# Performance work log

Hardware: AMD Instinct MI355X
Metric: run time of the kernel (lower is better)

The kernel has to match this reference:

```python
import jax, jax.numpy as jnp
import numpy as np

N = 100000          # number of active sparse points
GRID = 800          # coordinate grid extent (2D)
KS = 9              # 3x3 kernel offsets
C_IN = 24
C_HID = 144         # round(24 * 6)
C_OUT = 24
EPS = 1e-5


def _build_kernel_map():
    """Build MinkowskiEngine-style kernel map for a 3x3 stride-1 channelwise conv.
    Returns (in_idx, out_idx, off_id), each [KS*N] int32. Invalid (no neighbor)
    entries point to sentinel row N so the padded gather/scatter is a no-op."""
    rng = np.random.default_rng(0)
    flat = rng.choice(GRID * GRID, size=N, replace=False)  # unique 2D coords
    ys, xs = flat // GRID, flat % GRID
    coord_to_idx = -np.ones(GRID * GRID, dtype=np.int64)
    coord_to_idx[flat] = np.arange(N)
    in_chunks, out_chunks, off_chunks = [], [], []
    pts = np.arange(N, dtype=np.int64)
    k = 0
    for dy in (-1, 0, 1):
        for dx in (-1, 0, 1):
            ny, nx = ys + dy, xs + dx
            inside = (ny >= 0) & (ny < GRID) & (nx >= 0) & (nx < GRID)
            nflat = np.clip(ny, 0, GRID - 1) * GRID + np.clip(nx, 0, GRID - 1)
            nidx = np.where(inside, coord_to_idx[nflat], -1)
            valid = nidx >= 0
            in_chunks.append(np.where(valid, nidx, N))
            out_chunks.append(np.where(valid, pts, N))
            off_chunks.append(np.full(N, k, dtype=np.int64))
            k += 1
    in_idx = np.concatenate(in_chunks).astype(np.int32)
    out_idx = np.concatenate(out_chunks).astype(np.int32)
    off_id = np.concatenate(off_chunks).astype(np.int32)
    return in_idx, out_idx, off_id


def setup_inputs() -> dict:
    key = jax.random.key(0)
    ks = jax.random.split(key, 4)
    in_idx, out_idx, off_id = _build_kernel_map()
    return {
        "feats": jax.random.normal(ks[0], (N, C_IN), jnp.float32),
        "w1": jax.random.normal(ks[1], (C_IN, C_HID), jnp.float32) * 0.1,
        "g1": jnp.ones((C_HID,), jnp.float32),
        "b1": jnp.zeros((C_HID,), jnp.float32),
        "w2": jax.random.normal(ks[2], (KS, C_HID), jnp.float32) * 0.1,
        "g2": jnp.ones((C_HID,), jnp.float32),
        "b2": jnp.zeros((C_HID,), jnp.float32),
        "w3": jax.random.normal(ks[3], (C_HID, C_OUT), jnp.float32) * 0.1,
        "g3": jnp.ones((C_OUT,), jnp.float32),
        "b3": jnp.zeros((C_OUT,), jnp.float32),
        "in_idx": jnp.asarray(in_idx),
        "out_idx": jnp.asarray(out_idx),
        "off_id": jnp.asarray(off_id),
    }


def _bn(x, g, b):
    # MinkowskiBatchNorm forward (training mode): per-channel stats over points
    m = jnp.mean(x, axis=0)
    v = jnp.var(x, axis=0)
    return (x - m) * jax.lax.rsqrt(v + EPS) * g + b


def _relu6(x):
    return jnp.clip(x, 0.0, 6.0)


def _channelwise_conv3x3(x, w2, in_idx, out_idx, off_id):
    # gather-multiply-scatter: out[p, c] = sum_k w2[k, c] * x[nbr_k(p), c]
    xp = jnp.concatenate([x, jnp.zeros((1, x.shape[1]), x.dtype)], axis=0)  # sentinel row
    contrib = xp[in_idx] * w2[off_id]                     # [KS*N, C_HID]
    out = jnp.zeros((N + 1, x.shape[1]), x.dtype).at[out_idx].add(contrib)
    return out[:N]


def reference(feats, w1, g1, b1, w2, g2, b2, w3, g3, b3, in_idx, out_idx, off_id):
    x = _relu6(_bn(feats @ w1, g1, b1))                   # 1x1 expand
    x = _relu6(_bn(_channelwise_conv3x3(x, w2, in_idx, out_idx, off_id), g2, b2))
    x = _bn(x @ w3, g3, b3)                               # 1x1 project
    return x + feats                                      # residual (in==out, stride==1)
```

## Files before the change

### kernel.cpp

```cpp
#include <hip/hip_runtime.h>
#include <hip/hip_fp16.h>

#define N_PTS 100000
#define KSZ 9
#define C_IN 24
#define C_HID 144
#define C_OUT 24
#define EPSV 1e-5f

#define X1N_B 0ull
#define X2_B  28800512ull
#define ST_B  57600512ull
#define Y3_B  0ull

#define MU1_F  0
#define M1_F   32
#define SUM2_F 640
#define SQ2_F  800
#define SUM3_F 960
#define SQ3_F  992
#define ST_FLOATS 1024

typedef float f4v __attribute__((ext_vector_type(4)));

__device__ inline float4 f4z() { return make_float4(0.f, 0.f, 0.f, 0.f); }
__device__ inline float4 f4_fma_s(float s, float4 b, float4 c) {
    return make_float4(fmaf(s, b.x, c.x), fmaf(s, b.y, c.y),
                       fmaf(s, b.z, c.z), fmaf(s, b.w, c.w));
}
__device__ inline float clamp6(float x) { return fminf(fmaxf(x, 0.f), 6.f); }

__global__ void k_init(char* wsb) {
    int t = threadIdx.x;
    float* STF = (float*)(wsb + ST_B);
    for (int i = t; i < ST_FLOATS; i += 256) STF[i] = 0.f;
    float* sent = (float*)(wsb + X1N_B + (size_t)N_PTS * (C_HID * 2));
    if (t < 72) sent[t] = 0.f;
}

__global__ void k_moments(const float* __restrict__ feats, char* __restrict__ wsb) {
    int t = threadIdx.x;
    float* STF = (float*)(wsb + ST_B);
    int len = (N_PTS + gridDim.x - 1) / gridDim.x;
    int r0 = blockIdx.x * len;
    int r1 = min(r0 + len, N_PTS);
    if (t >= 600) return;
    float a = 0.f;
    if (t < 576) {
        int i = t / 24, j = t % 24;
#pragma unroll 4
        for (int r = r0; r < r1; r++)
            a = fmaf(feats[(size_t)r * 24 + i], feats[(size_t)r * 24 + j], a);
        atomicAdd(&STF[M1_F + t], a);
    } else {
        int k = t - 576;
#pragma unroll 4
        for (int r = r0; r < r1; r++) a += feats[(size_t)r * 24 + k];
        atomicAdd(&STF[MU1_F + k], a);
    }
}

__global__ void __launch_bounds__(576, 5)
k_gemm1(const float* __restrict__ feats, const float* __restrict__ w1,
        const float* __restrict__ g1, const float* __restrict__ b1,
        char* __restrict__ wsb) {
    __shared__ float scs[C_HID], shs[C_HID];
    float* STF = (float*)(wsb + ST_B);
    int t = threadIdx.x;
    if (t < C_HID) {
        float wc[C_IN];
#pragma unroll
        for (int k = 0; k < C_IN; k++) wc[k] = w1[k * C_HID + t];
        const float invN = 1.f / (float)N_PTS;
        float mean = 0.f;
#pragma unroll
        for (int k = 0; k < C_IN; k++) mean = fmaf(STF[MU1_F + k], wc[k], mean);
        mean *= invN;
        float e2 = 0.f;
        for (int i = 0; i < C_IN; i++) {
            float s = 0.f;
#pragma unroll
            for (int j = 0; j < C_IN; j++) s = fmaf(STF[M1_F + i * 24 + j], wc[j], s);
            e2 = fmaf(wc[i], s, e2);
        }
        e2 *= invN;
        float var = e2 - mean * mean;
        float s1 = g1[t] * rsqrtf(var + EPSV);
        scs[t] = s1;
        shs[t] = b1[t] - mean * s1;
    }
    __syncthreads();
    int c = t % C_HID, pg = t / C_HID;
    float sc = scs[c];
    float sh = shs[c];
    float wreg[C_IN];
#pragma unroll
    for (int k = 0; k < C_IN; k++) wreg[k] = w1[k * C_HID + c] * sc;
    __half* x1h = (__half*)(wsb + X1N_B);
    for (int p = blockIdx.x * 4 + pg; p < N_PTS; p += gridDim.x * 4) {
        const float4* fr = (const float4*)(feats + (size_t)p * C_IN);
        float acc = sh;
#pragma unroll
        for (int q = 0; q < 6; q++) {
            float4 f = fr[q];
            acc = fmaf(f.x, wreg[4 * q + 0], acc);
            acc = fmaf(f.y, wreg[4 * q + 1], acc);
            acc = fmaf(f.z, wreg[4 * q + 2], acc);
            acc = fmaf(f.w, wreg[4 * q + 3], acc);
        }
        x1h[(size_t)p * C_HID + c] = __float2half_rn(clamp6(acc));
    }
}

__global__ void k_conv(const float* __restrict__ w2, const int* __restrict__ in_idx,
                       char* __restrict__ wsb) {
    __shared__ float w2s[KSZ * C_HID];
    __shared__ float lsum[C_HID], lsq[C_HID];
    float* STF = (float*)(wsb + ST_B);
    int t = threadIdx.x;
    for (int e = t; e < KSZ * C_HID; e += 256) w2s[e] = w2[e];
    if (t < C_HID) { lsum[t] = 0.f; lsq[t] = 0.f; }
    __syncthreads();
    const __half* x1h = (const __half*)(wsb + X1N_B);
    __half* x2h = (__half*)(wsb + X2_B);
    const bool act = t < 252;
    int pt = t / 18, g = t % 18, c0 = g * 8;
    float rs[8], rq[8];
#pragma unroll
    for (int j = 0; j < 8; j++) { rs[j] = 0.f; rq[j] = 0.f; }
    const int nChunks = (N_PTS + 13) / 14;
    int ch = (int)blockIdx.x;
    int p = ch * 14 + pt;
    bool ok = act && p < N_PTS;
    int idxs[KSZ];
#pragma unroll
    for (int k = 0; k < KSZ; k++) idxs[k] = ok ? in_idx[k * N_PTS + p] : N_PTS;
    while (ch < nChunks) {
        float4 vv[KSZ];
#pragma unroll
        for (int k = 0; k < KSZ; k++)
            vv[k] = *(const float4*)(x1h + (size_t)idxs[k] * C_HID + c0);
        int chn = ch + (int)gridDim.x;
        int pn = chn * 14 + pt;
        bool okn = act && chn < nChunks && pn < N_PTS;
        int idxn[KSZ];
#pragma unroll
        for (int k = 0; k < KSZ; k++) idxn[k] = okn ? in_idx[k * N_PTS + pn] : N_PTS;
        float acc[8];
#pragma unroll
        for (int j = 0; j < 8; j++) acc[j] = 0.f;
#pragma unroll
        for (int k = 0; k < KSZ; k++) {
            union { float4 f; __half2 h[4]; } u;
            u.f = vv[k];
#pragma unroll
            for (int jj = 0; jj < 4; jj++) {
                float2 x = __half22float2(u.h[jj]);
                acc[2 * jj]     = fmaf(w2s[k * C_HID + c0 + 2 * jj],     x.x, acc[2 * jj]);
                acc[2 * jj + 1] = fmaf(w2s[k * C_HID + c0 + 2 * jj + 1], x.y, acc[2 * jj + 1]);
            }
        }
        if (ok) {
            union { f4v f; __half2 h[4]; } o;
#pragma unroll
            for (int jj = 0; jj < 4; jj++)
                o.h[jj] = __float22half2_rn(make_float2(acc[2 * jj], acc[2 * jj + 1]));
            __builtin_nontemporal_store(o.f, (f4v*)(x2h + (size_t)p * C_HID + c0));
#pragma unroll
            for (int j = 0; j < 8; j++) {
                rs[j] += acc[j];
                rq[j] = fmaf(acc[j], acc[j], rq[j]);
            }
        }
        ch = chn; p = pn; ok = okn;
#pragma unroll
        for (int k = 0; k < KSZ; k++) idxs[k] = idxn[k];
    }
    if (act) {
#pragma unroll
        for (int j = 0; j < 8; j++) {
            atomicAdd(&lsum[c0 + j], rs[j]);
            atomicAdd(&lsq[c0 + j], rq[j]);
        }
    }
    __syncthreads();
    if (t < C_HID) {
        atomicAdd(&STF[SUM2_F + t], lsum[t]);
        atomicAdd(&STF[SQ2_F + t], lsq[t]);
    }
}

__global__ void k_gemm2(const float* __restrict__ w3, const float* __restrict__ g2,
                        const float* __restrict__ b2, char* __restrict__ wsb) {
    __shared__ float4 w3s[C_HID * 6];
    __shared__ float4 sc2v[C_HID / 4], sh2v[C_HID / 4];
    float* STF = (float*)(wsb + ST_B);
    int t = threadIdx.x;
    for (int e = t; e < C_HID * 6; e += 256) w3s[e] = ((const float4*)w3)[e];
    if (t < C_HID) {
        const float invN = 1.f / (float)N_PTS;
        float mean = STF[SUM2_F + t] * invN;
        float var = STF[SQ2_F + t] * invN - mean * mean;
        float s = g2[t] * rsqrtf(var + EPSV);
        ((float*)sc2v)[t] = s;
        ((float*)sh2v)[t] = b2[t] - mean * s;
    }
    __syncthreads();
    int r = blockIdx.x * 256 + t;
    if (r >= N_PTS) return;
    const float4* x2v = (const float4*)(wsb + X2_B + (size_t)r * (C_HID * 2));
    float4 a[6];
#pragma unroll
    for (int c4 = 0; c4 < 6; c4++) a[c4] = f4z();
#pragma unroll 6
    for (int h8 = 0; h8 < 18; h8++) {
        union { float4 f; __half2 h[4]; } u;
        u.f = x2v[h8];
        float4 s0 = sc2v[2 * h8], s1 = sc2v[2 * h8 + 1];
        float4 b0 = sh2v[2 * h8], b1 = sh2v[2 * h8 + 1];
        float2 x0 = __half22float2(u.h[0]);
        float2 x1 = __half22float2(u.h[1]);
        float2 x2 = __half22float2(u.h[2]);
        float2 x3 = __half22float2(u.h[3]);
        float xs[8];
        xs[0] = clamp6(fmaf(x0.x, s0.x, b0.x));
        xs[1] = clamp6(fmaf(x0.y, s0.y, b0.y));
        xs[2] = clamp6(fmaf(x1.x, s0.z, b0.z));
        xs[3] = clamp6(fmaf(x1.y, s0.w, b0.w));
        xs[4] = clamp6(fmaf(x2.x, s1.x, b1.x));
        xs[5] = clamp6(fmaf(x2.y, s1.y, b1.y));
        xs[6] = clamp6(fmaf(x3.x, s1.z, b1.z));
        xs[7] = clamp6(fmaf(x3.y, s1.w, b1.w));
#pragma unroll
        for (int j = 0; j < 8; j++) {
            int h = h8 * 8 + j;
#pragma unroll
            for (int c4 = 0; c4 < 6; c4++)
                a[c4] = f4_fma_s(xs[j], w3s[h * 6 + c4], a[c4]);
        }
    }
    float4* y3v = (float4*)(wsb + Y3_B) + (size_t)r * 6;
#pragma unroll
    for (int c4 = 0; c4 < 6; c4++) y3v[c4] = a[c4];
}

__global__ void k_red3(char* __restrict__ wsb) {
    int t = threadIdx.x;
    const float* y3 = (const float*)(wsb + Y3_B);
    float* STF = (float*)(wsb + ST_B);
    float rs = 0.f, rq = 0.f;
    const int total = N_PTS * C_OUT;
    for (int e = blockIdx.x * 192 + t; e < total; e += gridDim.x * 192) {
        float v = y3[e];
        rs += v;
        rq = fmaf(v, v, rq);
    }
    __shared__ float ls[192], lq[192];
    ls[t] = rs; lq[t] = rq;
    __syncthreads();
    if (t < C_OUT) {
        float s = 0.f, q = 0.f;
        for (int u = t; u < 192; u += C_OUT) { s += ls[u]; q += lq[u]; }
        atomicAdd(&STF[SUM3_F + t], s);
        atomicAdd(&STF[SQ3_F + t], q);
    }
}

__global__ void k_out(const float* __restrict__ feats, const float* __restrict__ g3,
                      const float* __restrict__ b3, const char* __restrict__ wsb,
                      float* __restrict__ out) {
    __shared__ float s3[C_OUT], h3[C_OUT];
    const float* STF = (const float*)(wsb + ST_B);
    int t = threadIdx.x;
    if (t < C_OUT) {
        const float invN = 1.f / (float)N_PTS;
        float mean = STF[SUM3_F + t] * invN;
        float var = STF[SQ3_F + t] * invN - mean * mean;
        float s = g3[t] * rsqrtf(var + EPSV);
        s3[t] = s;
        h3[t] = b3[t] - mean * s;
    }
    __syncthreads();
    int tau = blockIdx.x * 256 + t;
    if (tau >= N_PTS * 6) return;
    int c = (tau % 6) * 4;
    float4 y = ((const float4*)(wsb + Y3_B))[tau];
    float4 f = ((const float4*)feats)[tau];
    float4 o;
    o.x = fmaf(y.x, s3[c + 0], h3[c + 0]) + f.x;
    o.y = fmaf(y.y, s3[c + 1], h3[c + 1]) + f.y;
    o.z = fmaf(y.z, s3[c + 2], h3[c + 2]) + f.z;
    o.w = fmaf(y.w, s3[c + 3], h3[c + 3]) + f.w;
    ((float4*)out)[tau] = o;
}

extern "C" void kernel_launch(void* const* d_in, const int* in_sizes, int n_in,
                              void* d_out, int out_size, void* d_ws, size_t ws_size,
                              hipStream_t stream) {
    const float* feats = (const float*)d_in[0];
    const float* w1 = (const float*)d_in[1];
    const float* g1 = (const float*)d_in[2];
    const float* b1 = (const float*)d_in[3];
    const float* w2 = (const float*)d_in[4];
    const float* g2 = (const float*)d_in[5];
    const float* b2 = (const float*)d_in[6];
    const float* w3 = (const float*)d_in[7];
    const float* g3 = (const float*)d_in[8];
    const float* b3 = (const float*)d_in[9];
    const int* in_idx = (const int*)d_in[10];
    char* wsb = (char*)d_ws;
    float* out = (float*)d_out;

    hipLaunchKernelGGL(k_init, dim3(1), dim3(256), 0, stream, wsb);
    hipLaunchKernelGGL(k_moments, dim3(256), dim3(640), 0, stream, feats, wsb);
    hipLaunchKernelGGL(k_gemm1, dim3(1024), dim3(576), 0, stream, feats, w1, g1, b1, wsb);
    hipLaunchKernelGGL(k_conv, dim3(2048), dim3(256), 0, stream, w2, in_idx, wsb);
    hipLaunchKernelGGL(k_gemm2, dim3((N_PTS + 255) / 256), dim3(256), 0, stream, w3, g2, b2, wsb);
    hipLaunchKernelGGL(k_red3, dim3(512), dim3(192), 0, stream, wsb);
    hipLaunchKernelGGL(k_out, dim3((N_PTS * 6 + 255) / 256), dim3(256), 0, stream,
                       feats, g3, b3, wsb, out);
}
```

Baseline: 292.6 us.

## Fuse all stages into one cooperative persistent kernel with grid syncs

```diff
diff --git a/kernel.cpp b/kernel.cpp
--- a/kernel.cpp
+++ b/kernel.cpp
@@ -1,5 +1,8 @@
 #include <hip/hip_runtime.h>
 #include <hip/hip_fp16.h>
+#include <hip/hip_cooperative_groups.h>
+
+namespace cg = cooperative_groups;
 
 #define N_PTS 100000
 #define KSZ 9
@@ -7,20 +10,30 @@
 #define C_HID 144
 #define C_OUT 24
 #define EPSV 1e-5f
+#define NB 768
+#define BT 256
+#define NCH14 ((N_PTS + 13) / 14)
+#define NPAIR (N_PTS / 2)
 
 #define X1N_B 0ull
 #define X2_B  28800512ull
 #define ST_B  57600512ull
 #define Y3_B  0ull
 
-#define MU1_F  0
-#define M1_F   32
-#define SUM2_F 640
-#define SQ2_F  800
-#define SUM3_F 960
-#define SQ3_F  992
-#define ST_FLOATS 1024
-
+#define MSUM1 0
+#define MSQ1  160
+#define MSUM2 320
+#define MSQ2  480
+#define MSUM3 640
+#define MSQ3  672
+#define FB_MU1  0
+#define FB_M1   32
+#define FB_SUM2 640
+#define FB_SQ2  800
+#define FB_SUM3 960
+#define FB_SQ3  992
+
+typedef float f2v __attribute__((ext_vector_type(2)));
 typedef float f4v __attribute__((ext_vector_type(4)));
 
 __device__ inline float4 f4z() { return make_float4(0.f, 0.f, 0.f, 0.f); }
@@ -30,12 +43,277 @@
 }
 __device__ inline float clamp6(float x) { return fminf(fmaxf(x, 0.f), 6.f); }
 
-__global__ void k_init(char* wsb) {
-    int t = threadIdx.x;
+__global__ void __launch_bounds__(BT, 4)
+mega(const float* __restrict__ feats, const float* __restrict__ w1,
+     const float* __restrict__ g1, const float* __restrict__ b1,
+     const float* __restrict__ w2, const float* __restrict__ g2,
+     const float* __restrict__ b2, const float* __restrict__ w3,
+     const float* __restrict__ g3, const float* __restrict__ b3,
+     const int* __restrict__ in_idx, char* __restrict__ wsb,
+     float* __restrict__ out) {
+    cg::grid_group gg = cg::this_grid();
+    __shared__ __align__(16) float smem[3936];
+    const int t = threadIdx.x;
+    const int bid = blockIdx.x;
     float* STF = (float*)(wsb + ST_B);
-    for (int i = t; i < ST_FLOATS; i += 256) STF[i] = 0.f;
-    float* sent = (float*)(wsb + X1N_B + (size_t)N_PTS * (C_HID * 2));
-    if (t < 72) sent[t] = 0.f;
+    __half* x1h = (__half*)(wsb + X1N_B);
+    __half* x2h = (__half*)(wsb + X2_B);
+
+    {
+        for (int e = t; e < 864; e += BT) ((float4*)smem)[e] = ((const float4*)w1)[e];
+        if (t < C_HID) { smem[3456 + t] = 0.f; smem[3600 + t] = 0.f; }
+        if (bid == 0 && t < 72)
+            ((unsigned int*)(x1h + (size_t)N_PTS * C_HID))[t] = 0xFC00FC00u;
+        __syncthreads();
+        const float4* w1s = (const float4*)smem;
+        bool act = t < 252;
+        int pt = t / 36, g = t % 36;
+        float4 rs = f4z(), rq = f4z();
+        for (int ch = bid; ch < NCH14; ch += NB) {
+            int pp = ch * 7 + pt;
+            if (act && pp < NPAIR) {
+                int p0 = pp * 2, p1 = p0 + 1;
+                const float4* fa = (const float4*)(feats + (size_t)p0 * C_IN);
+                const float4* fb = (const float4*)(feats + (size_t)p1 * C_IN);
+                float4 A = f4z(), Bv = f4z();
+#pragma unroll
+                for (int q = 0; q < 6; q++) {
+                    float4 x = fa[q], y = fb[q];
+                    float4 w0 = w1s[(4 * q + 0) * 36 + g];
+                    float4 w1r = w1s[(4 * q + 1) * 36 + g];
+                    float4 w2r = w1s[(4 * q + 2) * 36 + g];
+                    float4 w3r = w1s[(4 * q + 3) * 36 + g];
+                    A = f4_fma_s(x.x, w0, A);  Bv = f4_fma_s(y.x, w0, Bv);
+                    A = f4_fma_s(x.y, w1r, A); Bv = f4_fma_s(y.y, w1r, Bv);
+                    A = f4_fma_s(x.z, w2r, A); Bv = f4_fma_s(y.z, w2r, Bv);
+                    A = f4_fma_s(x.w, w3r, A); Bv = f4_fma_s(y.w, w3r, Bv);
+                }
+                union { f2v f; __half2 h2[2]; } ua, ub;
+                ua.h2[0] = __float22half2_rn(make_float2(A.x, A.y));
+                ua.h2[1] = __float22half2_rn(make_float2(A.z, A.w));
+                ub.h2[0] = __float22half2_rn(make_float2(Bv.x, Bv.y));
+                ub.h2[1] = __float22half2_rn(make_float2(Bv.z, Bv.w));
+                *(f2v*)(x1h + (size_t)p0 * C_HID + g * 4) = ua.f;
+                *(f2v*)(x1h + (size_t)p1 * C_HID + g * 4) = ub.f;
+                rs.x += A.x + Bv.x; rs.y += A.y + Bv.y;
+                rs.z += A.z + Bv.z; rs.w += A.w + Bv.w;
+                rq.x += A.x * A.x + Bv.x * Bv.x; rq.y += A.y * A.y + Bv.y * Bv.y;
+                rq.z += A.z * A.z + Bv.z * Bv.z; rq.w += A.w * A.w + Bv.w * Bv.w;
+            }
+        }
+        if (act) {
+            atomicAdd(&smem[3456 + g * 4 + 0], rs.x);
+            atomicAdd(&smem[3456 + g * 4 + 1], rs.y);
+            atomicAdd(&smem[3456 + g * 4 + 2], rs.z);
+            atomicAdd(&smem[3456 + g * 4 + 3], rs.w);
+            atomicAdd(&smem[3600 + g * 4 + 0], rq.x);
+            atomicAdd(&smem[3600 + g * 4 + 1], rq.y);
+            atomicAdd(&smem[3600 + g * 4 + 2], rq.z);
+            atomicAdd(&smem[3600 + g * 4 + 3], rq.w);
+        }
+        __syncthreads();
+        if (t < C_HID) {
+            atomicAdd(&STF[MSUM1 + t], smem[3456 + t]);
+            atomicAdd(&STF[MSQ1 + t], smem[3600 + t]);
+        }
+    }
+    __threadfence();
+    gg.sync();
+
+    {
+        for (int e = t; e < KSZ * C_HID; e += BT) smem[e] = w2[e];
+        if (t < C_HID) { smem[1296 + t] = 0.f; smem[1440 + t] = 0.f; }
+        bool act = t < 252;
+        int pt = t / 18, g = t % 18, c0 = g * 8;
+        float sc[8], sh[8];
+        const float invN = 1.f / (float)N_PTS;
+#pragma unroll
+        for (int j = 0; j < 8; j++) {
+            int c = c0 + j;
+            float mean = STF[MSUM1 + c] * invN;
+            float var = STF[MSQ1 + c] * invN - mean * mean;
+            float s = g1[c] * rsqrtf(var + EPSV);
+            sc[j] = s;
+            sh[j] = b1[c] - mean * s;
+        }
+        __syncthreads();
+        float rs[8], rq[8];
+#pragma unroll
+        for (int j = 0; j < 8; j++) { rs[j] = 0.f; rq[j] = 0.f; }
+        int ch = bid;
+        int p = ch * 14 + pt;
+        bool ok = act && p < N_PTS;
+        int idxs[KSZ];
+#pragma unroll
+        for (int k = 0; k < KSZ; k++) idxs[k] = ok ? in_idx[k * N_PTS + p] : N_PTS;
+        while (ch < NCH14) {
+            float4 vv[KSZ];
+#pragma unroll
+            for (int k = 0; k < KSZ; k++)
+                vv[k] = *(const float4*)(x1h + (size_t)idxs[k] * C_HID + c0);
+            int chn = ch + NB;
+            int pn = chn * 14 + pt;
+            bool okn = act && chn < NCH14 && pn < N_PTS;
+            int idxn[KSZ];
+#pragma unroll
+            for (int k = 0; k < KSZ; k++) idxn[k] = okn ? in_idx[k * N_PTS + pn] : N_PTS;
+            float acc[8];
+#pragma unroll
+            for (int j = 0; j < 8; j++) acc[j] = 0.f;
+#pragma unroll
+            for (int k = 0; k < KSZ; k++) {
+                union { float4 f; __half2 h[4]; } u;
+                u.f = vv[k];
+#pragma unroll
+                for (int jj = 0; jj < 4; jj++) {
+                    float2 x = __half22float2(u.h[jj]);
+                    float xa = clamp6(fmaf(x.x, sc[2 * jj], sh[2 * jj]));
+                    float xb = clamp6(fmaf(x.y, sc[2 * jj + 1], sh[2 * jj + 1]));
+                    acc[2 * jj]     = fmaf(smem[k * C_HID + c0 + 2 * jj], xa, acc[2 * jj]);
+                    acc[2 * jj + 1] = fmaf(smem[k * C_HID + c0 + 2 * jj + 1], xb, acc[2 * jj + 1]);
+                }
+            }
+            if (ok) {
+                union { f4v f; __half2 h[4]; } o;
+#pragma unroll
+                for (int jj = 0; jj < 4; jj++)
+                    o.h[jj] = __float22half2_rn(make_float2(acc[2 * jj], acc[2 * jj + 1]));
+                __builtin_nontemporal_store(o.f, (f4v*)(x2h + (size_t)p * C_HID + c0));
+            }
+#pragma unroll
+            for (int j = 0; j < 8; j++) {
+                rs[j] += acc[j];
+                rq[j] = fmaf(acc[j], acc[j], rq[j]);
+            }
+            ch = chn; p = pn; ok = okn;
+#pragma unroll
+            for (int k = 0; k < KSZ; k++) idxs[k] = idxn[k];
+        }
+        if (act) {
+#pragma unroll
+            for (int j = 0; j < 8; j++) {
+                atomicAdd(&smem[1296 + c0 + j], rs[j]);
+                atomicAdd(&smem[1440 + c0 + j], rq[j]);
+            }
+        }
+        __syncthreads();
+        if (t < C_HID) {
+            atomicAdd(&STF[MSUM2 + t], smem[1296 + t]);
+            atomicAdd(&STF[MSQ2 + t], smem[1440 + t]);
+        }
+    }
+    __threadfence();
+    gg.sync();
+
+    {
+        bool blkact = (bid * BT < N_PTS);
+        if (blkact) {
+            for (int e = t; e < 864; e += BT) ((float4*)smem)[e] = ((const float4*)w3)[e];
+            if (t < C_HID) {
+                const float invN = 1.f / (float)N_PTS;
+                float mean = STF[MSUM2 + t] * invN;
+                float var = STF[MSQ2 + t] * invN - mean * mean;
+                float s = g2[t] * rsqrtf(var + EPSV);
+                smem[3456 + t] = s;
+                smem[3600 + t] = b2[t] - mean * s;
+            }
+            __syncthreads();
+            int p = bid * BT + t;
+            bool ok = p < N_PTS;
+            float4 a[6];
+#pragma unroll
+            for (int c4 = 0; c4 < 6; c4++) a[c4] = f4z();
+            if (ok) {
+                const float4* xr = (const float4*)(x2h + (size_t)p * C_HID);
+                const float4* sc2 = (const float4*)(smem + 3456);
+                const float4* sh2 = (const float4*)(smem + 3600);
+                const float4* w3s = (const float4*)smem;
+#pragma unroll 3
+                for (int h8 = 0; h8 < 18; h8++) {
+                    union { float4 f; __half2 h[4]; } u;
+                    u.f = xr[h8];
+                    float4 s0 = sc2[2 * h8], s1 = sc2[2 * h8 + 1];
+                    float4 b0 = sh2[2 * h8], b1v = sh2[2 * h8 + 1];
+                    float2 x0 = __half22float2(u.h[0]);
+                    float2 x1 = __half22float2(u.h[1]);
+                    float2 x2 = __half22float2(u.h[2]);
+                    float2 x3 = __half22float2(u.h[3]);
+                    float xs[8];
+                    xs[0] = clamp6(fmaf(x0.x, s0.x, b0.x));
+                    xs[1] = clamp6(fmaf(x0.y, s0.y, b0.y));
+                    xs[2] = clamp6(fmaf(x1.x, s0.z, b0.z));
+                    xs[3] = clamp6(fmaf(x1.y, s0.w, b0.w));
+                    xs[4] = clamp6(fmaf(x2.x, s1.x, b1v.x));
+                    xs[5] = clamp6(fmaf(x2.y, s1.y, b1v.y));
+                    xs[6] = clamp6(fmaf(x3.x, s1.z, b1v.z));
+                    xs[7] = clamp6(fmaf(x3.y, s1.w, b1v.w));
+#pragma unroll
+                    for (int j = 0; j < 8; j++) {
+                        int h = h8 * 8 + j;
+#pragma unroll
+                        for (int c4 = 0; c4 < 6; c4++)
+                            a[c4] = f4_fma_s(xs[j], w3s[h * 6 + c4], a[c4]);
+                    }
+                }
+                float4* y3v = (float4*)(wsb + Y3_B) + (size_t)p * 6;
+#pragma unroll
+                for (int c4 = 0; c4 < 6; c4++) y3v[c4] = a[c4];
+            }
+            int wv = t >> 6, ln = t & 63;
+#pragma unroll
+            for (int c4 = 0; c4 < 6; c4++) {
+                float4 s = a[c4];
+                float4 q = make_float4(s.x * s.x, s.y * s.y, s.z * s.z, s.w * s.w);
+#pragma unroll
+                for (int m = 1; m < 64; m <<= 1) {
+                    s.x += __shfl_xor(s.x, m); s.y += __shfl_xor(s.y, m);
+                    s.z += __shfl_xor(s.z, m); s.w += __shfl_xor(s.w, m);
+                    q.x += __shfl_xor(q.x, m); q.y += __shfl_xor(q.y, m);
+                    q.z += __shfl_xor(q.z, m); q.w += __shfl_xor(q.w, m);
+                }
+                if (ln == 0) {
+                    int base = 3744 + wv * 48 + c4 * 4;
+                    smem[base + 0] = s.x; smem[base + 1] = s.y;
+                    smem[base + 2] = s.z; smem[base + 3] = s.w;
+                    smem[base + 24 + 0] = q.x; smem[base + 24 + 1] = q.y;
+                    smem[base + 24 + 2] = q.z; smem[base + 24 + 3] = q.w;
+                }
+            }
+            __syncthreads();
+            if (t < 48) {
+                float v = smem[3744 + t] + smem[3744 + 48 + t] +
+                          smem[3744 + 96 + t] + smem[3744 + 144 + t];
+                if (t < 24) atomicAdd(&STF[MSUM3 + t], v);
+                else        atomicAdd(&STF[MSQ3 + t - 24], v);
+            }
+        }
+    }
+    __threadfence();
+    gg.sync();
+
+    {
+        if (t < C_OUT) {
+            const float invN = 1.f / (float)N_PTS;
+            float mean = STF[MSUM3 + t] * invN;
+            float var = STF[MSQ3 + t] * invN - mean * mean;
+            float s = g3[t] * rsqrtf(var + EPSV);
+            smem[t] = s;
+            smem[32 + t] = b3[t] - mean * s;
+        }
+        __syncthreads();
+        const float4* s3v = (const float4*)smem;
+        const float4* h3v = (const float4*)(smem + 32);
+        const int T = N_PTS * 6;
+        for (int tau = bid * BT + t; tau < T; tau += NB * BT) {
+            int c4 = tau % 6;
+            float4 y = ((const float4*)(wsb + Y3_B))[tau];
+            float4 f = ((const float4*)feats)[tau];
+            float4 s = s3v[c4], h = h3v[c4];
+            ((float4*)out)[tau] = make_float4(
+                fmaf(y.x, s.x, h.x) + f.x, fmaf(y.y, s.y, h.y) + f.y,
+                fmaf(y.z, s.z, h.z) + f.z, fmaf(y.w, s.w, h.w) + f.w);
+        }
+    }
 }
 
 __global__ void k_moments(const float* __restrict__ feats, char* __restrict__ wsb) {
@@ -51,12 +329,12 @@
 #pragma unroll 4
         for (int r = r0; r < r1; r++)
             a = fmaf(feats[(size_t)r * 24 + i], feats[(size_t)r * 24 + j], a);
-        atomicAdd(&STF[M1_F + t], a);
+        atomicAdd(&STF[FB_M1 + t], a);
     } else {
         int k = t - 576;
 #pragma unroll 4
         for (int r = r0; r < r1; r++) a += feats[(size_t)r * 24 + k];
-        atomicAdd(&STF[MU1_F + k], a);
+        atomicAdd(&STF[FB_MU1 + k], a);
     }
 }
 
@@ -74,13 +352,13 @@
         const float invN = 1.f / (float)N_PTS;
         float mean = 0.f;
 #pragma unroll
-        for (int k = 0; k < C_IN; k++) mean = fmaf(STF[MU1_F + k], wc[k], mean);
+        for (int k = 0; k < C_IN; k++) mean = fmaf(STF[FB_MU1 + k], wc[k], mean);
         mean *= invN;
         float e2 = 0.f;
         for (int i = 0; i < C_IN; i++) {
             float s = 0.f;
 #pragma unroll
-            for (int j = 0; j < C_IN; j++) s = fmaf(STF[M1_F + i * 24 + j], wc[j], s);
+            for (int j = 0; j < C_IN; j++) s = fmaf(STF[FB_M1 + i * 24 + j], wc[j], s);
             e2 = fmaf(wc[i], s, e2);
         }
         e2 *= invN;
@@ -112,8 +390,8 @@
     }
 }
 
-__global__ void k_conv(const float* __restrict__ w2, const int* __restrict__ in_idx,
-                       char* __restrict__ wsb) {
+__global__ void k_conv_fb(const float* __restrict__ w2, const int* __restrict__ in_idx,
+                          char* __restrict__ wsb) {
     __shared__ float w2s[KSZ * C_HID];
     __shared__ float lsum[C_HID], lsq[C_HID];
     float* STF = (float*)(wsb + ST_B);
@@ -128,21 +406,20 @@
     float rs[8], rq[8];
 #pragma unroll
     for (int j = 0; j < 8; j++) { rs[j] = 0.f; rq[j] = 0.f; }
-    const int nChunks = (N_PTS + 13) / 14;
     int ch = (int)blockIdx.x;
     int p = ch * 14 + pt;
     bool ok = act && p < N_PTS;
     int idxs[KSZ];
 #pragma unroll
     for (int k = 0; k < KSZ; k++) idxs[k] = ok ? in_idx[k * N_PTS + p] : N_PTS;
-    while (ch < nChunks) {
+    while (ch < NCH14) {
         float4 vv[KSZ];
 #pragma unroll
         for (int k = 0; k < KSZ; k++)
             vv[k] = *(const float4*)(x1h + (size_t)idxs[k] * C_HID + c0);
         int chn = ch + (int)gridDim.x;
         int pn = chn * 14 + pt;
-        bool okn = act && chn < nChunks && pn < N_PTS;
+        bool okn = act && chn < NCH14 && pn < N_PTS;
         int idxn[KSZ];
 #pragma unroll
         for (int k = 0; k < KSZ; k++) idxn[k] = okn ? in_idx[k * N_PTS + pn] : N_PTS;
@@ -151,12 +428,12 @@
         for (int j = 0; j < 8; j++) acc[j] = 0.f;
 #pragma unroll
         for (int k = 0; k < KSZ; k++) {
-            union { float4 f; __half2 h[4]; } u;
+            union { float4 f; __half2 h[2][2]; } u;
             u.f = vv[k];
 #pragma unroll
             for (int jj = 0; jj < 4; jj++) {
-                float2 x = __half22float2(u.h[jj]);
-                acc[2 * jj]     = fmaf(w2s[k * C_HID + c0 + 2 * jj],     x.x, acc[2 * jj]);
+                float2 x = __half22float2(u.h[jj >> 1][jj & 1]);
+                acc[2 * jj]     = fmaf(w2s[k * C_HID + c0 + 2 * jj], x.x, acc[2 * jj]);
                 acc[2 * jj + 1] = fmaf(w2s[k * C_HID + c0 + 2 * jj + 1], x.y, acc[2 * jj + 1]);
             }
         }
@@ -166,11 +443,11 @@
             for (int jj = 0; jj < 4; jj++)
                 o.h[jj] = __float22half2_rn(make_float2(acc[2 * jj], acc[2 * jj + 1]));
             __builtin_nontemporal_store(o.f, (f4v*)(x2h + (size_t)p * C_HID + c0));
-#pragma unroll
-            for (int j = 0; j < 8; j++) {
-                rs[j] += acc[j];
-                rq[j] = fmaf(acc[j], acc[j], rq[j]);
-            }
+        }
+#pragma unroll
+        for (int j = 0; j < 8; j++) {
+            rs[j] += acc[j];
+            rq[j] = fmaf(acc[j], acc[j], rq[j]);
         }
         ch = chn; p = pn; ok = okn;
 #pragma unroll
@@ -185,8 +462,8 @@
     }
     __syncthreads();
     if (t < C_HID) {
-        atomicAdd(&STF[SUM2_F + t], lsum[t]);
-        atomicAdd(&STF[SQ2_F + t], lsq[t]);
+        atomicAdd(&STF[FB_SUM2 + t], lsum[t]);
+        atomicAdd(&STF[FB_SQ2 + t], lsq[t]);
     }
 }
 
@@ -194,75 +471,82 @@
                         const float* __restrict__ b2, char* __restrict__ wsb) {
     __shared__ float4 w3s[C_HID * 6];
     __shared__ float4 sc2v[C_HID / 4], sh2v[C_HID / 4];
+    __shared__ float red[192];
     float* STF = (float*)(wsb + ST_B);
     int t = threadIdx.x;
     for (int e = t; e < C_HID * 6; e += 256) w3s[e] = ((const float4*)w3)[e];
     if (t < C_HID) {
         const float invN = 1.f / (float)N_PTS;
-        float mean = STF[SUM2_F + t] * invN;
-        float var = STF[SQ2_F + t] * invN - mean * mean;
+        float mean = STF[FB_SUM2 + t] * invN;
+        float var = STF[FB_SQ2 + t] * invN - mean * mean;
         float s = g2[t] * rsqrtf(var + EPSV);
         ((float*)sc2v)[t] = s;
         ((float*)sh2v)[t] = b2[t] - mean * s;
     }
     __syncthreads();
     int r = blockIdx.x * 256 + t;
-    if (r >= N_PTS) return;
-    const float4* x2v = (const float4*)(wsb + X2_B + (size_t)r * (C_HID * 2));
+    bool ok = r < N_PTS;
     float4 a[6];
 #pragma unroll
     for (int c4 = 0; c4 < 6; c4++) a[c4] = f4z();
-#pragma unroll 6
-    for (int h8 = 0; h8 < 18; h8++) {
-        union { float4 f; __half2 h[4]; } u;
-        u.f = x2v[h8];
-        float4 s0 = sc2v[2 * h8], s1 = sc2v[2 * h8 + 1];
-        float4 b0 = sh2v[2 * h8], b1 = sh2v[2 * h8 + 1];
-        float2 x0 = __half22float2(u.h[0]);
-        float2 x1 = __half22float2(u.h[1]);
-        float2 x2 = __half22float2(u.h[2]);
-        float2 x3 = __half22float2(u.h[3]);
-        float xs[8];
-        xs[0] = clamp6(fmaf(x0.x, s0.x, b0.x));
-        xs[1] = clamp6(fmaf(x0.y, s0.y, b0.y));
-        xs[2] = clamp6(fmaf(x1.x, s0.z, b0.z));
-        xs[3] = clamp6(fmaf(x1.y, s0.w, b0.w));
-        xs[4] = clamp6(fmaf(x2.x, s1.x, b1.x));
-        xs[5] = clamp6(fmaf(x2.y, s1.y, b1.y));
-        xs[6] = clamp6(fmaf(x3.x, s1.z, b1.z));
-        xs[7] = clamp6(fmaf(x3.y, s1.w, b1.w));
-#pragma unroll
-        for (int j = 0; j < 8; j++) {
-            int h = h8 * 8 + j;
-#pragma unroll
-            for (int c4 = 0; c4 < 6; c4++)
-                a[c4] = f4_fma_s(xs[j], w3s[h * 6 + c4], a[c4]);
-        }
-    }
-    float4* y3v = (float4*)(wsb + Y3_B) + (size_t)r * 6;
-#pragma unroll
-    for (int c4 = 0; c4 < 6; c4++) y3v[c4] = a[c4];
-}
-
-__global__ void k_red3(char* __restrict__ wsb) {
-    int t = threadIdx.x;
-    const float* y3 = (const float*)(wsb + Y3_B);
-    float* STF = (float*)(wsb + ST_B);
-    float rs = 0.f, rq = 0.f;
-    const int total = N_PTS * C_OUT;
-    for (int e = blockIdx.x * 192 + t; e < total; e += gridDim.x * 192) {
-        float v = y3[e];
-        rs += v;
-        rq = fmaf(v, v, rq);
-    }
-    __shared__ float ls[192], lq[192];
-    ls[t] = rs; lq[t] = rq;
+    if (ok) {
+        const float4* x2v = (const float4*)(wsb + X2_B + (size_t)r * (C_HID * 2));
+#pragma unroll 3
+        for (int h8 = 0; h8 < 18; h8++) {
+            union { float4 f; __half2 h[4]; } u;
+            u.f = x2v[h8];
+            float4 s0 = sc2v[2 * h8], s1 = sc2v[2 * h8 + 1];
+            float4 b0 = sh2v[2 * h8], b1v = sh2v[2 * h8 + 1];
+            float2 x0 = __half22float2(u.h[0]);
+            float2 x1 = __half22float2(u.h[1]);
+            float2 x2 = __half22float2(u.h[2]);
+            float2 x3 = __half22float2(u.h[3]);
+            float xs[8];
+            xs[0] = clamp6(fmaf(x0.x, s0.x, b0.x));
+            xs[1] = clamp6(fmaf(x0.y, s0.y, b0.y));
+            xs[2] = clamp6(fmaf(x1.x, s0.z, b0.z));
+            xs[3] = clamp6(fmaf(x1.y, s0.w, b0.w));
+            xs[4] = clamp6(fmaf(x2.x, s1.x, b1v.x));
+            xs[5] = clamp6(fmaf(x2.y, s1.y, b1v.y));
+            xs[6] = clamp6(fmaf(x3.x, s1.z, b1v.z));
+            xs[7] = clamp6(fmaf(x3.y, s1.w, b1v.w));
+#pragma unroll
+            for (int j = 0; j < 8; j++) {
+                int h = h8 * 8 + j;
+#pragma unroll
+                for (int c4 = 0; c4 < 6; c4++)
+                    a[c4] = f4_fma_s(xs[j], w3s[h * 6 + c4], a[c4]);
+            }
+        }
+        float4* y3v = (float4*)(wsb + Y3_B) + (size_t)r * 6;
+#pragma unroll
+        for (int c4 = 0; c4 < 6; c4++) y3v[c4] = a[c4];
+    }
+    int wv = t >> 6, ln = t & 63;
+#pragma unroll
+    for (int c4 = 0; c4 < 6; c4++) {
+        float4 s = a[c4];
+        float4 q = make_float4(s.x * s.x, s.y * s.y, s.z * s.z, s.w * s.w);
+#pragma unroll
+        for (int m = 1; m < 64; m <<= 1) {
+            s.x += __shfl_xor(s.x, m); s.y += __shfl_xor(s.y, m);
+            s.z += __shfl_xor(s.z, m); s.w += __shfl_xor(s.w, m);
+            q.x += __shfl_xor(q.x, m); q.y += __shfl_xor(q.y, m);
+            q.z += __shfl_xor(q.z, m); q.w += __shfl_xor(q.w, m);
+        }
+        if (ln == 0) {
+            int base = wv * 48 + c4 * 4;
+            red[base + 0] = s.x; red[base + 1] = s.y;
+            red[base + 2] = s.z; red[base + 3] = s.w;
+            red[base + 24 + 0] = q.x; red[base + 24 + 1] = q.y;
+            red[base + 24 + 2] = q.z; red[base + 24 + 3] = q.w;
+        }
+    }
     __syncthreads();
-    if (t < C_OUT) {
-        float s = 0.f, q = 0.f;
-        for (int u = t; u < 192; u += C_OUT) { s += ls[u]; q += lq[u]; }
-        atomicAdd(&STF[SUM3_F + t], s);
-        atomicAdd(&STF[SQ3_F + t], q);
+    if (t < 48) {
+        float v = red[t] + red[48 + t] + red[96 + t] + red[144 + t];
+        if (t < 24) atomicAdd(&STF[FB_SUM3 + t], v);
+        else        atomicAdd(&STF[FB_SQ3 + t - 24], v);
     }
 }
 
@@ -274,8 +558,8 @@
     int t = threadIdx.x;
     if (t < C_OUT) {
         const float invN = 1.f / (float)N_PTS;
-        float mean = STF[SUM3_F + t] * invN;
-        float var = STF[SQ3_F + t] * invN - mean * mean;
+        float mean = STF[FB_SUM3 + t] * invN;
+        float var = STF[FB_SQ3 + t] * invN - mean * mean;
         float s = g3[t] * rsqrtf(var + EPSV);
         s3[t] = s;
         h3[t] = b3[t] - mean * s;
@@ -311,12 +595,37 @@
     char* wsb = (char*)d_ws;
     float* out = (float*)d_out;
 
-    hipLaunchKernelGGL(k_init, dim3(1), dim3(256), 0, stream, wsb);
-    hipLaunchKernelGGL(k_moments, dim3(256), dim3(640), 0, stream, feats, wsb);
-    hipLaunchKernelGGL(k_gemm1, dim3(1024), dim3(576), 0, stream, feats, w1, g1, b1, wsb);
-    hipLaunchKernelGGL(k_conv, dim3(2048), dim3(256), 0, stream, w2, in_idx, wsb);
-    hipLaunchKernelGGL(k_gemm2, dim3((N_PTS + 255) / 256), dim3(256), 0, stream, w3, g2, b2, wsb);
-    hipLaunchKernelGGL(k_red3, dim3(512), dim3(192), 0, stream, wsb);
-    hipLaunchKernelGGL(k_out, dim3((N_PTS * 6 + 255) / 256), dim3(256), 0, stream,
-                       feats, g3, b3, wsb, out);
-}
+    (void)hipMemsetAsync(wsb + ST_B, 0, 4096, stream);
+    (void)hipMemsetAsync(wsb + (size_t)N_PTS * C_HID * 2, 0, C_HID * 2, stream);
+
+    static int coop_ok = -1;
+    if (coop_ok < 0) {
+        int nblk = 0, ncu = 0, dev = 0;
+        (void)hipGetDevice(&dev);
+        hipError_t e1 = hipOccupancyMaxActiveBlocksPerMultiprocessor(
+            &nblk, (const void*)mega, BT, 0);
+        hipError_t e2 = hipDeviceGetAttribute(
+            &ncu, hipDeviceAttributeMultiprocessorCount, dev);
+        coop_ok = (e1 == hipSuccess && e2 == hipSuccess && nblk * ncu >= NB) ? 1 : 0;
+    }
+
+    bool did_coop = false;
+    if (coop_ok) {
+        void* args[] = {(void*)&feats, (void*)&w1, (void*)&g1, (void*)&b1,
+                        (void*)&w2, (void*)&g2, (void*)&b2, (void*)&w3,
+                        (void*)&g3, (void*)&b3, (void*)&in_idx, (void*)&wsb,
+                        (void*)&out};
+        hipError_t e = hipLaunchCooperativeKernel((const void*)mega, dim3(NB), dim3(BT),
+                                                  args, 0, stream);
+        did_coop = (e == hipSuccess);
+    }
+    if (!did_coop) {
+        hipLaunchKernelGGL(k_moments, dim3(256), dim3(640), 0, stream, feats, wsb);
+        hipLaunchKernelGGL(k_gemm1, dim3(1024), dim3(576), 0, stream, feats, w1, g1, b1, wsb);
+        hipLaunchKernelGGL(k_conv_fb, dim3(2048), dim3(256), 0, stream, w2, in_idx, wsb);
+        hipLaunchKernelGGL(k_gemm2, dim3((N_PTS + 255) / 256), dim3(256), 0, stream,
+                           w3, g2, b2, wsb);
+        hipLaunchKernelGGL(k_out, dim3((N_PTS * 6 + 255) / 256), dim3(256), 0, stream,
+                           feats, g3, b3, wsb, out);
+    }
+}
```

Result: slower. 313.6 us (+7.2%).

## Defer BN1 into conv gather, fuse output stats into gemm2, drop moment kernels

Applied to the files above, without the earlier changes.

```diff
diff --git a/kernel.cpp b/kernel.cpp
--- a/kernel.cpp
+++ b/kernel.cpp
@@ -7,20 +7,22 @@
 #define C_HID 144
 #define C_OUT 24
 #define EPSV 1e-5f
+#define NCH14 ((N_PTS + 13) / 14)
+#define NPAIR (N_PTS / 2)
 
 #define X1N_B 0ull
 #define X2_B  28800512ull
 #define ST_B  57600512ull
 #define Y3_B  0ull
 
-#define MU1_F  0
-#define M1_F   32
-#define SUM2_F 640
-#define SQ2_F  800
-#define SUM3_F 960
-#define SQ3_F  992
-#define ST_FLOATS 1024
-
+#define MSUM1 0
+#define MSQ1  160
+#define MSUM2 320
+#define MSQ2  480
+#define MSUM3 640
+#define MSQ3  672
+
+typedef float f2v __attribute__((ext_vector_type(2)));
 typedef float f4v __attribute__((ext_vector_type(4)));
 
 __device__ inline float4 f4z() { return make_float4(0.f, 0.f, 0.f, 0.f); }
@@ -30,89 +32,74 @@
 }
 __device__ inline float clamp6(float x) { return fminf(fmaxf(x, 0.f), 6.f); }
 
-__global__ void k_init(char* wsb) {
-    int t = threadIdx.x;
+__global__ void __launch_bounds__(256)
+k_gemm1(const float* __restrict__ feats, const float* __restrict__ w1,
+        char* __restrict__ wsb) {
+    __shared__ __align__(16) float smem[3744];
     float* STF = (float*)(wsb + ST_B);
-    for (int i = t; i < ST_FLOATS; i += 256) STF[i] = 0.f;
-    float* sent = (float*)(wsb + X1N_B + (size_t)N_PTS * (C_HID * 2));
-    if (t < 72) sent[t] = 0.f;
-}
-
-__global__ void k_moments(const float* __restrict__ feats, char* __restrict__ wsb) {
-    int t = threadIdx.x;
-    float* STF = (float*)(wsb + ST_B);
-    int len = (N_PTS + gridDim.x - 1) / gridDim.x;
-    int r0 = blockIdx.x * len;
-    int r1 = min(r0 + len, N_PTS);
-    if (t >= 600) return;
-    float a = 0.f;
-    if (t < 576) {
-        int i = t / 24, j = t % 24;
-#pragma unroll 4
-        for (int r = r0; r < r1; r++)
-            a = fmaf(feats[(size_t)r * 24 + i], feats[(size_t)r * 24 + j], a);
-        atomicAdd(&STF[M1_F + t], a);
-    } else {
-        int k = t - 576;
-#pragma unroll 4
-        for (int r = r0; r < r1; r++) a += feats[(size_t)r * 24 + k];
-        atomicAdd(&STF[MU1_F + k], a);
-    }
-}
-
-__global__ void __launch_bounds__(576, 5)
-k_gemm1(const float* __restrict__ feats, const float* __restrict__ w1,
-        const float* __restrict__ g1, const float* __restrict__ b1,
-        char* __restrict__ wsb) {
-    __shared__ float scs[C_HID], shs[C_HID];
-    float* STF = (float*)(wsb + ST_B);
-    int t = threadIdx.x;
+    __half* x1h = (__half*)(wsb + X1N_B);
+    const int t = threadIdx.x;
+    const int bid = blockIdx.x;
+    for (int e = t; e < 864; e += 256) ((float4*)smem)[e] = ((const float4*)w1)[e];
+    if (t < C_HID) { smem[3456 + t] = 0.f; smem[3600 + t] = 0.f; }
+    if (bid == 0 && t < 72)
+        ((unsigned int*)(x1h + (size_t)N_PTS * C_HID))[t] = 0xFC00FC00u;
+    __syncthreads();
+    const float4* w1s = (const float4*)smem;
+    bool act = t < 252;
+    int pt = t / 36, g = t % 36;
+    float4 rs = f4z(), rq = f4z();
+    for (int ch = bid; ch < NCH14; ch += (int)gridDim.x) {
+        int pp = ch * 7 + pt;
+        if (act && pp < NPAIR) {
+            int p0 = pp * 2, p1 = p0 + 1;
+            const float4* fa = (const float4*)(feats + (size_t)p0 * C_IN);
+            const float4* fb = (const float4*)(feats + (size_t)p1 * C_IN);
+            float4 A = f4z(), Bv = f4z();
+#pragma unroll
+            for (int q = 0; q < 6; q++) {
+                float4 x = fa[q], y = fb[q];
+                float4 w0 = w1s[(4 * q + 0) * 36 + g];
+                float4 w1r = w1s[(4 * q + 1) * 36 + g];
+                float4 w2r = w1s[(4 * q + 2) * 36 + g];
+                float4 w3r = w1s[(4 * q + 3) * 36 + g];
+                A = f4_fma_s(x.x, w0, A);  Bv = f4_fma_s(y.x, w0, Bv);
+                A = f4_fma_s(x.y, w1r, A); Bv = f4_fma_s(y.y, w1r, Bv);
+                A = f4_fma_s(x.z, w2r, A); Bv = f4_fma_s(y.z, w2r, Bv);
+                A = f4_fma_s(x.w, w3r, A); Bv = f4_fma_s(y.w, w3r, Bv);
+            }
+            union { f2v f; __half2 h2[2]; } ua, ub;
+            ua.h2[0] = __float22half2_rn(make_float2(A.x, A.y));
+            ua.h2[1] = __float22half2_rn(make_float2(A.z, A.w));
+            ub.h2[0] = __float22half2_rn(make_float2(Bv.x, Bv.y));
+            ub.h2[1] = __float22half2_rn(make_float2(Bv.z, Bv.w));
+            *(f2v*)(x1h + (size_t)p0 * C_HID + g * 4) = ua.f;
+            *(f2v*)(x1h + (size_t)p1 * C_HID + g * 4) = ub.f;
+            rs.x += A.x + Bv.x; rs.y += A.y + Bv.y;
+            rs.z += A.z + Bv.z; rs.w += A.w + Bv.w;
+            rq.x += A.x * A.x + Bv.x * Bv.x; rq.y += A.y * A.y + Bv.y * Bv.y;
+            rq.z += A.z * A.z + Bv.z * Bv.z; rq.w += A.w * A.w + Bv.w * Bv.w;
+        }
+    }
+    if (act) {
+        atomicAdd(&smem[3456 + g * 4 + 0], rs.x);
+        atomicAdd(&smem[3456 + g * 4 + 1], rs.y);
+        atomicAdd(&smem[3456 + g * 4 + 2], rs.z);
+        atomicAdd(&smem[3456 + g * 4 + 3], rs.w);
+        atomicAdd(&smem[3600 + g * 4 + 0], rq.x);
+        atomicAdd(&smem[3600 + g * 4 + 1], rq.y);
+        atomicAdd(&smem[3600 + g * 4 + 2], rq.z);
+        atomicAdd(&smem[3600 + g * 4 + 3], rq.w);
+    }
+    __syncthreads();
     if (t < C_HID) {
-        float wc[C_IN];
-#pragma unroll
-        for (int k = 0; k < C_IN; k++) wc[k] = w1[k * C_HID + t];
-        const float invN = 1.f / (float)N_PTS;
-        float mean = 0.f;
-#pragma unroll
-        for (int k = 0; k < C_IN; k++) mean = fmaf(STF[MU1_F + k], wc[k], mean);
-        mean *= invN;
-        float e2 = 0.f;
-        for (int i = 0; i < C_IN; i++) {
-            float s = 0.f;
-#pragma unroll
-            for (int j = 0; j < C_IN; j++) s = fmaf(STF[M1_F + i * 24 + j], wc[j], s);
-            e2 = fmaf(wc[i], s, e2);
-        }
-        e2 *= invN;
-        float var = e2 - mean * mean;
-        float s1 = g1[t] * rsqrtf(var + EPSV);
-        scs[t] = s1;
-        shs[t] = b1[t] - mean * s1;
-    }
-    __syncthreads();
-    int c = t % C_HID, pg = t / C_HID;
-    float sc = scs[c];
-    float sh = shs[c];
-    float wreg[C_IN];
-#pragma unroll
-    for (int k = 0; k < C_IN; k++) wreg[k] = w1[k * C_HID + c] * sc;
-    __half* x1h = (__half*)(wsb + X1N_B);
-    for (int p = blockIdx.x * 4 + pg; p < N_PTS; p += gridDim.x * 4) {
-        const float4* fr = (const float4*)(feats + (size_t)p * C_IN);
-        float acc = sh;
-#pragma unroll
-        for (int q = 0; q < 6; q++) {
-            float4 f = fr[q];
-            acc = fmaf(f.x, wreg[4 * q + 0], acc);
-            acc = fmaf(f.y, wreg[4 * q + 1], acc);
-            acc = fmaf(f.z, wreg[4 * q + 2], acc);
-            acc = fmaf(f.w, wreg[4 * q + 3], acc);
-        }
-        x1h[(size_t)p * C_HID + c] = __float2half_rn(clamp6(acc));
-    }
-}
-
-__global__ void k_conv(const float* __restrict__ w2, const int* __restrict__ in_idx,
+        atomicAdd(&STF[MSUM1 + t], smem[3456 + t]);
+        atomicAdd(&STF[MSQ1 + t], smem[3600 + t]);
+    }
+}
+
+__global__ void k_conv(const float* __restrict__ w2, const float* __restrict__ g1,
+                       const float* __restrict__ b1, const int* __restrict__ in_idx,
                        char* __restrict__ wsb) {
     __shared__ float w2s[KSZ * C_HID];
     __shared__ float lsum[C_HID], lsq[C_HID];
@@ -120,29 +107,41 @@
     int t = threadIdx.x;
     for (int e = t; e < KSZ * C_HID; e += 256) w2s[e] = w2[e];
     if (t < C_HID) { lsum[t] = 0.f; lsq[t] = 0.f; }
+    const bool act = t < 252;
+    int pt = t / 18, g = t % 18, c0 = g * 8;
+    float sc[8], sh[8];
+    {
+        const float invN = 1.f / (float)N_PTS;
+#pragma unroll
+        for (int j = 0; j < 8; j++) {
+            int c = c0 + j;
+            float mean = STF[MSUM1 + c] * invN;
+            float var = STF[MSQ1 + c] * invN - mean * mean;
+            float s = g1[c] * rsqrtf(var + EPSV);
+            sc[j] = s;
+            sh[j] = b1[c] - mean * s;
+        }
+    }
     __syncthreads();
     const __half* x1h = (const __half*)(wsb + X1N_B);
     __half* x2h = (__half*)(wsb + X2_B);
-    const bool act = t < 252;
-    int pt = t / 18, g = t % 18, c0 = g * 8;
     float rs[8], rq[8];
 #pragma unroll
     for (int j = 0; j < 8; j++) { rs[j] = 0.f; rq[j] = 0.f; }
-    const int nChunks = (N_PTS + 13) / 14;
     int ch = (int)blockIdx.x;
     int p = ch * 14 + pt;
     bool ok = act && p < N_PTS;
     int idxs[KSZ];
 #pragma unroll
     for (int k = 0; k < KSZ; k++) idxs[k] = ok ? in_idx[k * N_PTS + p] : N_PTS;
-    while (ch < nChunks) {
+    while (ch < NCH14) {
         float4 vv[KSZ];
 #pragma unroll
         for (int k = 0; k < KSZ; k++)
             vv[k] = *(const float4*)(x1h + (size_t)idxs[k] * C_HID + c0);
         int chn = ch + (int)gridDim.x;
         int pn = chn * 14 + pt;
-        bool okn = act && chn < nChunks && pn < N_PTS;
+        bool okn = act && chn < NCH14 && pn < N_PTS;
         int idxn[KSZ];
 #pragma unroll
         for (int k = 0; k < KSZ; k++) idxn[k] = okn ? in_idx[k * N_PTS + pn] : N_PTS;
@@ -156,8 +155,10 @@
 #pragma unroll
             for (int jj = 0; jj < 4; jj++) {
                 float2 x = __half22float2(u.h[jj]);
-                acc[2 * jj]     = fmaf(w2s[k * C_HID + c0 + 2 * jj],     x.x, acc[2 * jj]);
-                acc[2 * jj + 1] = fmaf(w2s[k * C_HID + c0 + 2 * jj + 1], x.y, acc[2 * jj + 1]);
+                float xa = clamp6(fmaf(x.x, sc[2 * jj], sh[2 * jj]));
+                float xb = clamp6(fmaf(x.y, sc[2 * jj + 1], sh[2 * jj + 1]));
+                acc[2 * jj]     = fmaf(w2s[k * C_HID + c0 + 2 * jj], xa, acc[2 * jj]);
+                acc[2 * jj + 1] = fmaf(w2s[k * C_HID + c0 + 2 * jj + 1], xb, acc[2 * jj + 1]);
             }
         }
         if (ok) {
@@ -166,11 +167,11 @@
             for (int jj = 0; jj < 4; jj++)
                 o.h[jj] = __float22half2_rn(make_float2(acc[2 * jj], acc[2 * jj + 1]));
             __builtin_nontemporal_store(o.f, (f4v*)(x2h + (size_t)p * C_HID + c0));
-#pragma unroll
-            for (int j = 0; j < 8; j++) {
-                rs[j] += acc[j];
-                rq[j] = fmaf(acc[j], acc[j], rq[j]);
-            }
+        }
+#pragma unroll
+        for (int j = 0; j < 8; j++) {
+            rs[j] += acc[j];
+            rq[j] = fmaf(acc[j], acc[j], rq[j]);
         }
         ch = chn; p = pn; ok = okn;
 #pragma unroll
@@ -185,8 +186,8 @@
     }
     __syncthreads();
     if (t < C_HID) {
-        atomicAdd(&STF[SUM2_F + t], lsum[t]);
-        atomicAdd(&STF[SQ2_F + t], lsq[t]);
+        atomicAdd(&STF[MSUM2 + t], lsum[t]);
+        atomicAdd(&STF[MSQ2 + t], lsq[t]);
     }
 }
 
@@ -194,75 +195,82 @@
                         const float* __restrict__ b2, char* __restrict__ wsb) {
     __shared__ float4 w3s[C_HID * 6];
     __shared__ float4 sc2v[C_HID / 4], sh2v[C_HID / 4];
+    __shared__ float red[192];
     float* STF = (float*)(wsb + ST_B);
     int t = threadIdx.x;
     for (int e = t; e < C_HID * 6; e += 256) w3s[e] = ((const float4*)w3)[e];
     if (t < C_HID) {
         const float invN = 1.f / (float)N_PTS;
-        float mean = STF[SUM2_F + t] * invN;
-        float var = STF[SQ2_F + t] * invN - mean * mean;
+        float mean = STF[MSUM2 + t] * invN;
+        float var = STF[MSQ2 + t] * invN - mean * mean;
         float s = g2[t] * rsqrtf(var + EPSV);
         ((float*)sc2v)[t] = s;
         ((float*)sh2v)[t] = b2[t] - mean * s;
     }
     __syncthreads();
     int r = blockIdx.x * 256 + t;
-    if (r >= N_PTS) return;
-    const float4* x2v = (const float4*)(wsb + X2_B + (size_t)r * (C_HID * 2));
+    bool ok = r < N_PTS;
     float4 a[6];
 #pragma unroll
     for (int c4 = 0; c4 < 6; c4++) a[c4] = f4z();
-#pragma unroll 6
-    for (int h8 = 0; h8 < 18; h8++) {
-        union { float4 f; __half2 h[4]; } u;
-        u.f = x2v[h8];
-        float4 s0 = sc2v[2 * h8], s1 = sc2v[2 * h8 + 1];
-        float4 b0 = sh2v[2 * h8], b1 = sh2v[2 * h8 + 1];
-        float2 x0 = __half22float2(u.h[0]);
-        float2 x1 = __half22float2(u.h[1]);
-        float2 x2 = __half22float2(u.h[2]);
-        float2 x3 = __half22float2(u.h[3]);
-        float xs[8];
-        xs[0] = clamp6(fmaf(x0.x, s0.x, b0.x));
-        xs[1] = clamp6(fmaf(x0.y, s0.y, b0.y));
-        xs[2] = clamp6(fmaf(x1.x, s0.z, b0.z));
-        xs[3] = clamp6(fmaf(x1.y, s0.w, b0.w));
-        xs[4] = clamp6(fmaf(x2.x, s1.x, b1.x));
-        xs[5] = clamp6(fmaf(x2.y, s1.y, b1.y));
-        xs[6] = clamp6(fmaf(x3.x, s1.z, b1.z));
-        xs[7] = clamp6(fmaf(x3.y, s1.w, b1.w));
-#pragma unroll
-        for (int j = 0; j < 8; j++) {
-            int h = h8 * 8 + j;
-#pragma unroll
-            for (int c4 = 0; c4 < 6; c4++)
-                a[c4] = f4_fma_s(xs[j], w3s[h * 6 + c4], a[c4]);
-        }
-    }
-    float4* y3v = (float4*)(wsb + Y3_B) + (size_t)r * 6;
-#pragma unroll
-    for (int c4 = 0; c4 < 6; c4++) y3v[c4] = a[c4];
-}
-
-__global__ void k_red3(char* __restrict__ wsb) {
-    int t = threadIdx.x;
-    const float* y3 = (const float*)(wsb + Y3_B);
-    float* STF = (float*)(wsb + ST_B);
-    float rs = 0.f, rq = 0.f;
-    const int total = N_PTS * C_OUT;
-    for (int e = blockIdx.x * 192 + t; e < total; e += gridDim.x * 192) {
-        float v = y3[e];
-        rs += v;
-        rq = fmaf(v, v, rq);
-    }
-    __shared__ float ls[192], lq[192];
-    ls[t] = rs; lq[t] = rq;
-    __syncthreads();
-    if (t < C_OUT) {
-        float s = 0.f, q = 0.f;
-        for (int u = t; u < 192; u += C_OUT) { s += ls[u]; q += lq[u]; }
-        atomicAdd(&STF[SUM3_F + t], s);
-        atomicAdd(&STF[SQ3_F + t], q);
+    if (ok) {
+        const float4* x2v = (const float4*)(wsb + X2_B + (size_t)r * (C_HID * 2));
+#pragma unroll 3
+        for (int h8 = 0; h8 < 18; h8++) {
+            union { float4 f; __half2 h[4]; } u;
+            u.f = x2v[h8];
+            float4 s0 = sc2v[2 * h8], s1 = sc2v[2 * h8 + 1];
+            float4 b0 = sh2v[2 * h8], b1v = sh2v[2 * h8 + 1];
+            float2 x0 = __half22float2(u.h[0]);
+            float2 x1 = __half22float2(u.h[1]);
+            float2 x2 = __half22float2(u.h[2]);
+            float2 x3 = __half22float2(u.h[3]);
+            float xs[8];
+            xs[0] = clamp6(fmaf(x0.x, s0.x, b0.x));
+            xs[1] = clamp6(fmaf(x0.y, s0.y, b0.y));
+            xs[2] = clamp6(fmaf(x1.x, s0.z, b0.z));
+            xs[3] = clamp6(fmaf(x1.y, s0.w, b0.w));
+            xs[4] = clamp6(fmaf(x2.x, s1.x, b1v.x));
+            xs[5] = clamp6(fmaf(x2.y, s1.y, b1v.y));
+            xs[6] = clamp6(fmaf(x3.x, s1.z, b1v.z));
+            xs[7] = clamp6(fmaf(x3.y, s1.w, b1v.w));
+#pragma unroll
+            for (int j = 0; j < 8; j++) {
+                int h = h8 * 8 + j;
+#pragma unroll
+                for (int c4 = 0; c4 < 6; c4++)
+                    a[c4] = f4_fma_s(xs[j], w3s[h * 6 + c4], a[c4]);
+            }
+        }
+        float4* y3v = (float4*)(wsb + Y3_B) + (size_t)r * 6;
+#pragma unroll
+        for (int c4 = 0; c4 < 6; c4++) y3v[c4] = a[c4];
+    }
+    int wv = t >> 6, ln = t & 63;
+#pragma unroll
+    for (int c4 = 0; c4 < 6; c4++) {
+        float4 s = a[c4];
+        float4 q = make_float4(s.x * s.x, s.y * s.y, s.z * s.z, s.w * s.w);
+#pragma unroll
+        for (int m = 1; m < 64; m <<= 1) {
+            s.x += __shfl_xor(s.x, m); s.y += __shfl_xor(s.y, m);
+            s.z += __shfl_xor(s.z, m); s.w += __shfl_xor(s.w, m);
+            q.x += __shfl_xor(q.x, m); q.y += __shfl_xor(q.y, m);
+            q.z += __shfl_xor(q.z, m); q.w += __shfl_xor(q.w, m);
+        }
+        if (ln == 0) {
+            int base = wv * 48 + c4 * 4;
+            red[base + 0] = s.x; red[base + 1] = s.y;
+            red[base + 2] = s.z; red[base + 3] = s.w;
+            red[base + 24 + 0] = q.x; red[base + 24 + 1] = q.y;
+            red[base + 24 + 2] = q.z; red[base + 24 + 3] = q.w;
+        }
+    }
+    __syncthreads();
+    if (t < 48) {
+        float v = red[t] + red[48 + t] + red[96 + t] + red[144 + t];
+        if (t < 24) atomicAdd(&STF[MSUM3 + t], v);
+        else        atomicAdd(&STF[MSQ3 + t - 24], v);
     }
 }
 
@@ -274,8 +282,8 @@
     int t = threadIdx.x;
     if (t < C_OUT) {
         const float invN = 1.f / (float)N_PTS;
-        float mean = STF[SUM3_F + t] * invN;
-        float var = STF[SQ3_F + t] * invN - mean * mean;
+        float mean = STF[MSUM3 + t] * invN;
+        float var = STF[MSQ3 + t] * invN - mean * mean;
         float s = g3[t] * rsqrtf(var + EPSV);
         s3[t] = s;
         h3[t] = b3[t] - mean * s;
@@ -311,12 +319,11 @@
     char* wsb = (char*)d_ws;
     float* out = (float*)d_out;
 
-    hipLaunchKernelGGL(k_init, dim3(1), dim3(256), 0, stream, wsb);
-    hipLaunchKernelGGL(k_moments, dim3(256), dim3(640), 0, stream, feats, wsb);
-    hipLaunchKernelGGL(k_gemm1, dim3(1024), dim3(576), 0, stream, feats, w1, g1, b1, wsb);
-    hipLaunchKernelGGL(k_conv, dim3(2048), dim3(256), 0, stream, w2, in_idx, wsb);
-    hipLaunchKernelGGL(k_gemm2, dim3((N_PTS + 255) / 256), dim3(256), 0, stream, w3, g2, b2, wsb);
-    hipLaunchKernelGGL(k_red3, dim3(512), dim3(192), 0, stream, wsb);
+    (void)hipMemsetAsync(wsb + ST_B, 0, 4096, stream);
+    hipLaunchKernelGGL(k_gemm1, dim3(2048), dim3(256), 0, stream, feats, w1, wsb);
+    hipLaunchKernelGGL(k_conv, dim3(2048), dim3(256), 0, stream, w2, g1, b1, in_idx, wsb);
+    hipLaunchKernelGGL(k_gemm2, dim3((N_PTS + 255) / 256), dim3(256), 0, stream,
+                       w3, g2, b2, wsb);
     hipLaunchKernelGGL(k_out, dim3((N_PTS * 6 + 255) / 256), dim3(256), 0, stream,
                        feats, g3, b3, wsb, out);
 }
```

After: 377.5 us. 1.29x slower.
